# Kernel optimization log

Hardware: AMD Instinct MI355X
Metric: run time of the kernel (lower is better)

The kernel has to match this reference:

```python
import jax, jax.numpy as jnp
import numpy as np

N = 50000      # nodes
E = 800000     # edges (avg degree 16)
D = 128        # input_nf = output_nf
H = 128        # hidden_nf


def _lin_init(key, fan_in, fan_out, gain=1.0):
    return gain * jax.random.normal(key, (fan_in, fan_out), jnp.float32) / np.sqrt(fan_in)


def setup_inputs() -> dict:
    key = jax.random.key(0)
    ks = jax.random.split(key, 20)
    h = jax.random.normal(ks[0], (N, D), jnp.float32)
    coord_diff = 0.5 * jax.random.normal(ks[1], (E, 3), jnp.float32)
    row = jax.random.randint(ks[2], (E,), 0, N, jnp.int32)
    col = jax.random.randint(ks[3], (E,), 0, N, jnp.int32)
    return {
        "h": h, "coord_diff": coord_diff, "row": row, "col": col,
        # edge_nn: Linear(2D+1 -> H), SiLU, Linear(H -> H), SiLU
        "We1": _lin_init(ks[4], 2 * D + 1, H), "be1": jnp.zeros((H,), jnp.float32),
        "We2": _lin_init(ks[5], H, H),          "be2": jnp.zeros((H,), jnp.float32),
        # node_nn: Linear(H+D -> H), SiLU, Linear(H -> D)
        "Wn1": _lin_init(ks[6], H + D, H), "bn1": jnp.zeros((H,), jnp.float32),
        "Wn2": _lin_init(ks[7], H, D),     "bn2": jnp.zeros((D,), jnp.float32),
        # coord_nn: Linear(H -> H), SiLU, Linear(H -> 1, no bias, gain 0.001)
        "Wc1": _lin_init(ks[8], H, H), "bc1": jnp.zeros((H,), jnp.float32),
        "Wc2": _lin_init(ks[9], H, 1, gain=0.001),
        # vel_scaling_nn: Linear(D -> H), SiLU, Linear(H -> 1)
        "Wv1": _lin_init(ks[10], D, H), "bv1": jnp.zeros((H,), jnp.float32),
        "Wv2": _lin_init(ks[11], H, 1), "bv2": jnp.zeros((1,), jnp.float32),
    }


def reference(h, coord_diff, row, col,
              We1, be1, We2, be2,
              Wn1, bn1, Wn2, bn2,
              Wc1, bc1, Wc2,
              Wv1, bv1, Wv2, bv2):
    n = h.shape[0]
    silu = jax.nn.silu
    # radial: squared edge length, [E,1]
    radial = jnp.sum(coord_diff * coord_diff, axis=1, keepdims=True)
    # edge model: gather endpoint features + radial, 2-layer SiLU MLP
    e_in = jnp.concatenate([h[row], h[col], radial], axis=1)        # [E, 2D+1]
    m = silu(silu(e_in @ We1 + be1) @ We2 + be2)                    # [E, H]
    # force model: per-edge scalar coefficient, clamped scatter-mean (coords_weight=1.0)
    coef = silu(m @ Wc1 + bc1) @ Wc2                                # [E, 1]
    trans = jnp.clip(coord_diff * coef, -100.0, 100.0)              # [E, 3]
    f_sum = jax.ops.segment_sum(trans, row, num_segments=n)         # [N, 3]
    cnt = jax.ops.segment_sum(jnp.ones((trans.shape[0], 1), trans.dtype), row, num_segments=n)
    force = f_sum / jnp.clip(cnt, 1.0)                              # segment mean, count clamped >=1
    # node model: scatter-sum of edge messages, then 2-layer MLP
    agg = jax.ops.segment_sum(m, row, num_segments=n)               # [N, H]
    h_cat = jnp.concatenate([h, agg], axis=1)                       # [N, D+H]
    h_out = silu(h_cat @ Wn1 + bn1) @ Wn2 + bn2                     # [N, D]
    # velocity scaling head
    vel = silu(h @ Wv1 + bv1) @ Wv2 + bv2                           # [N, 1]
    return (vel, force, h_out)
```

## Files before the change

### kernel.cpp

```cpp
#include <hip/hip_runtime.h>

#define NN 50000
#define EE 800000

typedef unsigned short u16;
typedef unsigned int u32;
typedef __attribute__((ext_vector_type(8))) short short8;
typedef __attribute__((ext_vector_type(4))) float f32x4;
typedef __attribute__((ext_vector_type(2))) float f32x2;

__device__ __forceinline__ u16 f2bf(float f) {
    union { float f; u32 i; } v; v.f = f;
    u32 x = v.i;
    return (u16)((x + 0x7fffu + ((x >> 16) & 1u)) >> 16);
}
__device__ __forceinline__ u32 pkr(float lo, float hi) {
    union { float f; u32 i; } a, b; a.f = lo; b.f = hi;
    return __builtin_amdgcn_perm(b.i + 0x8000u, a.i + 0x8000u, 0x07060302u);
}
__device__ __forceinline__ float bf2f(short x) {
    union { u32 i; float f; } v; v.i = ((u32)(u16)x) << 16; return v.f;
}
__device__ __forceinline__ float siluf(float x) {
    return x * __builtin_amdgcn_rcpf(1.0f + __expf(-x));
}
__device__ __forceinline__ void atomic_pk_add_bf16(u16* addr, u32 data) {
    asm volatile("global_atomic_pk_add_bf16 %0, %1, off" :: "v"(addr), "v"(data) : "memory");
}

__device__ __forceinline__ int b_idx2(int k, int n) {
    int chunk = ((k >> 5) << 3) + ((n >> 5) << 1) + (n & 1);
    return chunk * 512 + (((k >> 3) & 3) << 7) + (((n >> 1) & 15) << 3) + (k & 7);
}

__global__ __launch_bounds__(256) void prep_kernel(
    const float* __restrict__ We1, const float* __restrict__ We2,
    const float* __restrict__ Wc1, const float* __restrict__ Wn1,
    const float* __restrict__ Wn2, const float* __restrict__ Wv1,
    u16* __restrict__ We1bf, u16* __restrict__ We2bf, u16* __restrict__ Wc1bf,
    u16* __restrict__ Wn1bf, u16* __restrict__ Wn2bf, u16* __restrict__ Wv1bf)
{
    int i = blockIdx.x * 256 + threadIdx.x;
    if (i < 32768) {
        int k = i >> 7, n = i & 127;
        We1bf[b_idx2(k, n)] = f2bf(We1[k * 128 + n]);
    } else if (i < 49152) {
        int t = i - 32768; int k = t >> 7, n = t & 127;
        We2bf[b_idx2(k, n)] = f2bf(We2[k * 128 + n]);
    } else if (i < 65536) {
        int t = i - 49152; int k = t >> 7, n = t & 127;
        Wc1bf[b_idx2(k, n)] = f2bf(Wc1[k * 128 + n]);
    } else if (i < 98304) {
        int t = i - 65536; int k = t >> 7, n = t & 127;
        Wn1bf[b_idx2(k, n)] = f2bf(Wn1[k * 128 + n]);
    } else if (i < 114688) {
        int t = i - 98304; int k = t >> 7, n = t & 127;
        Wn2bf[b_idx2(k, n)] = f2bf(Wn2[k * 128 + n]);
    } else {
        int t = i - 114688; int k = t >> 7, n = t & 127;
        Wv1bf[b_idx2(k, n)] = f2bf(Wv1[k * 128 + n]);
    }
}

__global__ __launch_bounds__(256) void hist_kernel(const int* __restrict__ row,
                                                   u32* __restrict__ bins)
{
    int e = blockIdx.x * 256 + threadIdx.x;
    if (e < EE) atomicAdd(&bins[row[e]], 1u);
}

__global__ __launch_bounds__(256) void scan1_kernel(const u32* __restrict__ bins,
                                                    u32* __restrict__ part)
{
    __shared__ u32 wsum[4];
    int i = blockIdx.x * 256 + threadIdx.x;
    u32 v = (i < NN) ? bins[i] : 0u;
    #pragma unroll
    for (int o = 1; o < 64; o <<= 1) v += __shfl_xor(v, o);
    if ((threadIdx.x & 63) == 0) wsum[threadIdx.x >> 6] = v;
    __syncthreads();
    if (threadIdx.x == 0) part[blockIdx.x] = wsum[0] + wsum[1] + wsum[2] + wsum[3];
}

__global__ __launch_bounds__(256) void scan2_kernel(u32* __restrict__ part, int np)
{
    __shared__ u32 s[256];
    int t = threadIdx.x;
    s[t] = (t < np) ? part[t] : 0u;
    __syncthreads();
    if (t == 0) {
        u32 run = 0;
        for (int i = 0; i < 256; ++i) { u32 x = s[i]; s[i] = run; run += x; }
    }
    __syncthreads();
    if (t < np) part[t] = s[t];
}

__global__ __launch_bounds__(256) void scan3_kernel(const u32* __restrict__ bins,
                                                    const u32* __restrict__ part,
                                                    u32* __restrict__ cursor)
{
    __shared__ u32 wsum[4];
    int t = threadIdx.x;
    int i = blockIdx.x * 256 + t;
    u32 v = (i < NN) ? bins[i] : 0u;
    u32 x = v;
    #pragma unroll
    for (int o = 1; o < 64; o <<= 1) {
        u32 y = __shfl_up(x, o);
        if ((t & 63) >= o) x += y;
    }
    if ((t & 63) == 63) wsum[t >> 6] = x;
    __syncthreads();
    u32 base = part[blockIdx.x];
    for (int wv = 0; wv < (t >> 6); ++wv) base += wsum[wv];
    if (i < NN) cursor[i] = base + x - v;
}

__global__ __launch_bounds__(256) void scatter_kernel(
    const int* __restrict__ row, const int* __restrict__ col,
    const float* __restrict__ cdiff, u32* __restrict__ cursor,
    u32* __restrict__ edata)
{
    int e = blockIdx.x * 256 + threadIdx.x;
    if (e < EE) {
        int r = row[e];
        u32 p = atomicAdd(&cursor[r], 1u);
        float cx = cdiff[(size_t)e * 3 + 0];
        float cy = cdiff[(size_t)e * 3 + 1];
        float cz = cdiff[(size_t)e * 3 + 2];
        float rad = cx * cx + cy * cy + cz * cz;
        uint4 ed;
        ed.x = (u32)r;
        ed.y = (u32)col[e];
        ed.z = __float_as_uint(rad);
        ed.w = (u32)e;
        *(uint4*)(edata + (size_t)p * 4) = ed;
    }
}

__global__ __launch_bounds__(256, 4) void pgemm_kernel(
    const float* __restrict__ h, const float* __restrict__ be1,
    const u16* __restrict__ We1bf,
    u16* __restrict__ P1bf, u16* __restrict__ P2bf,
    u16* __restrict__ hbf, u32 use_hbf)
{
    __shared__ u16 sX[8192];

    const int tid = threadIdx.x;
    const int nblk = blockIdx.x * 64;
    const int w = tid >> 6;
    const int lane = tid & 63;
    const int m15 = lane & 15, q = lane >> 4;
    const int n0 = w * 32 + 2 * m15, n1 = n0 + 1;
    const int ard = (m15 + 64 * q) * 8;
    const float b0 = be1[n0], b1 = be1[n1];

    {
        int r = tid & 63, j = tid >> 6;
        int n = nblk + r; if (n > NN - 1) n = NN - 1;
        const float* src = h + (size_t)n * 128 + j * 32;
        #pragma unroll
        for (int i = 0; i < 4; ++i) {
            float4 a = *(const float4*)(src + i * 8);
            float4 b = *(const float4*)(src + i * 8 + 4);
            int slot = r + ((j * 4 + i) << 6);
            uint4 v = make_uint4(pkr(a.x, a.y), pkr(a.z, a.w),
                                 pkr(b.x, b.y), pkr(b.z, b.w));
            *(uint4*)&sX[slot * 8] = v;
            if (use_hbf)
                *(uint4*)(hbf + (size_t)n * 128 + j * 32 + i * 8) = v;
        }
    }
    __syncthreads();

    f32x4 acc[4][2];

    #pragma unroll
    for (int mt = 0; mt < 4; ++mt)
        #pragma unroll
        for (int r = 0; r < 4; ++r) { acc[mt][0][r] = b0; acc[mt][1][r] = b1; }
    #pragma unroll
    for (int c = 0; c < 4; ++c) {
        short8 bf0 = *(const short8*)(We1bf + (c * 8 + w * 2 + 0) * 512 + lane * 8);
        short8 bf1 = *(const short8*)(We1bf + (c * 8 + w * 2 + 1) * 512 + lane * 8);
        #pragma unroll
        for (int mt = 0; mt < 4; ++mt) {
            short8 af = *(const short8*)(sX + ard + c * 2048 + mt * 128);
            acc[mt][0] = __builtin_amdgcn_mfma_f32_16x16x32_bf16(af, bf0, acc[mt][0], 0, 0, 0);
            acc[mt][1] = __builtin_amdgcn_mfma_f32_16x16x32_bf16(af, bf1, acc[mt][1], 0, 0, 0);
        }
    }
    #pragma unroll
    for (int mt = 0; mt < 4; ++mt)
        #pragma unroll
        for (int r = 0; r < 4; ++r) {
            int n = nblk + mt * 16 + q * 4 + r;
            if (n < NN)
                *(u32*)(P1bf + (size_t)n * 128 + n0) = pkr(acc[mt][0][r], acc[mt][1][r]);
        }

    #pragma unroll
    for (int mt = 0; mt < 4; ++mt)
        #pragma unroll
        for (int r = 0; r < 4; ++r) { acc[mt][0][r] = 0.0f; acc[mt][1][r] = 0.0f; }
    #pragma unroll
    for (int c = 4; c < 8; ++c) {
        short8 bf0 = *(const short8*)(We1bf + (c * 8 + w * 2 + 0) * 512 + lane * 8);
        short8 bf1 = *(const short8*)(We1bf + (c * 8 + w * 2 + 1) * 512 + lane * 8);
        #pragma unroll
        for (int mt = 0; mt < 4; ++mt) {
            short8 af = *(const short8*)(sX + ard + (c - 4) * 2048 + mt * 128);
            acc[mt][0] = __builtin_amdgcn_mfma_f32_16x16x32_bf16(af, bf0, acc[mt][0], 0, 0, 0);
            acc[mt][1] = __builtin_amdgcn_mfma_f32_16x16x32_bf16(af, bf1, acc[mt][1], 0, 0, 0);
        }
    }
    #pragma unroll
    for (int mt = 0; mt < 4; ++mt)
        #pragma unroll
        for (int r = 0; r < 4; ++r) {
            int n = nblk + mt * 16 + q * 4 + r;
            if (n < NN)
                *(u32*)(P2bf + (size_t)n * 128 + n0) = pkr(acc[mt][0][r], acc[mt][1][r]);
        }
}

__global__ __launch_bounds__(256, 8) void edge_kernel(
    const u16* __restrict__ P1bf, const u16* __restrict__ P2bf,
    const float* __restrict__ cdiff,
    const u32* __restrict__ edata,
    const float* __restrict__ We1,
    const float* __restrict__ be2, const float* __restrict__ bc1,
    const float* __restrict__ Wc2,
    const u16* __restrict__ We2bf, const u16* __restrict__ Wc1bf,
    u16* __restrict__ aggbf, float* __restrict__ fsum)
{
    __shared__ u16 sT[8192];
    __shared__ int sRow[64];
    __shared__ int sEg[64];
    __shared__ int sRid[64];
    __shared__ float sCoefP[4][64];
    __shared__ float sF[192];

    const int tid = threadIdx.x;
    const int e0 = blockIdx.x * 64;
    const int w = tid >> 6;
    const int lane = tid & 63;
    const int m15 = lane & 15, q = lane >> 4;
    const int n0 = w * 32 + 2 * m15, n1 = n0 + 1;
    const int lsw = (lane ^ q) * 8;
    const int a_ = m15 >> 2;
    const int sbase = (a_ << 7) + (q << 5) + ((m15 & 3) << 1);
    const int o0 = (0 ^ a_) << 3, o1 = (1 ^ a_) << 3, o2 = (2 ^ a_) << 3, o3 = (3 ^ a_) << 3;

    const float b2a = be2[n0], b2b = be2[n1];
    const float b3a = bc1[n0], b3b = bc1[n1];
    const float wc2a = Wc2[n0], wc2b = Wc2[n1];

    {
        int e = tid & 63, seg = tid >> 6;
        uint4 ed = *(const uint4*)(edata + (size_t)(e0 + e) * 4);
        int nr = (int)ed.x, nc = (int)ed.y;
        float rad = __uint_as_float(ed.z);
        if (seg == 0) { sRow[e] = nr; sEg[e] = (int)ed.w; }
        const u16* p1 = P1bf + (size_t)nr * 128 + seg * 32;
        const u16* p2 = P2bf + (size_t)nc * 128 + seg * 32;
        const float* wr = We1 + 256 * 128 + seg * 32;
        u16* tb = sT + (((seg * 4 + (e >> 4)) << 9) + (((e >> 2) & 3) << 5));
        const int rl = e & 3;
        #pragma unroll 2
        for (int g = 0; g < 4; ++g) {
            short8 x1 = *(const short8*)(p1 + g * 8);
            short8 x2 = *(const short8*)(p2 + g * 8);
            float4 wa = *(const float4*)(wr + g * 8);
            float4 wb = *(const float4*)(wr + g * 8 + 4);
            float v[8];
            #pragma unroll
            for (int t = 0; t < 4; ++t) {
                v[t]     = siluf(bf2f(x1[t])     + bf2f(x2[t])     + rad * ((const float*)&wa)[t]);
                v[t + 4] = siluf(bf2f(x1[t + 4]) + bf2f(x2[t + 4]) + rad * ((const float*)&wb)[t]);
            }
            uint4 dd = make_uint4(pkr(v[0], v[1]), pkr(v[2], v[3]),
                                  pkr(v[4], v[5]), pkr(v[6], v[7]));
            *(uint4*)(tb + ((g << 7) + ((rl ^ g) << 3))) = dd;
        }
    }
    __syncthreads();

    if (tid < 64) {
        int e = tid;
        int head = (e == 0) || (sRow[e] != sRow[e - 1]);
        int v = head ? e : 0;
        #pragma unroll
        for (int o = 1; o < 64; o <<= 1) {
            int y = __shfl_up(v, o);
            if (e >= o && y > v) v = y;
        }
        sRid[e] = v;
        sF[e * 3 + 0] = 0.f; sF[e * 3 + 1] = 0.f; sF[e * 3 + 2] = 0.f;
    }

    f32x4 acc[4][2];
    u32 d[4][4];

    #pragma unroll
    for (int mt = 0; mt < 4; ++mt)
        #pragma unroll
        for (int r = 0; r < 4; ++r) { acc[mt][0][r] = b2a; acc[mt][1][r] = b2b; }
    #pragma unroll
    for (int c = 0; c < 4; ++c) {
        short8 bf0 = *(const short8*)(We2bf + (c * 8 + w * 2 + 0) * 512 + lane * 8);
        short8 bf1 = *(const short8*)(We2bf + (c * 8 + w * 2 + 1) * 512 + lane * 8);
        #pragma unroll
        for (int mt = 0; mt < 4; ++mt) {
            short8 af = *(const short8*)(sT + (c * 4 + mt) * 512 + lsw);
            acc[mt][0] = __builtin_amdgcn_mfma_f32_16x16x32_bf16(af, bf0, acc[mt][0], 0, 0, 0);
            acc[mt][1] = __builtin_amdgcn_mfma_f32_16x16x32_bf16(af, bf1, acc[mt][1], 0, 0, 0);
        }
    }
    #pragma unroll
    for (int mt = 0; mt < 4; ++mt)
        #pragma unroll
        for (int r = 0; r < 4; ++r)
            d[mt][r] = pkr(siluf(acc[mt][0][r]), siluf(acc[mt][1][r]));
    __syncthreads();
    #pragma unroll
    for (int mt = 0; mt < 4; ++mt) {
        u16* bp = sT + (w * 4 + mt) * 512 + sbase;
        *(u32*)(bp + o0) = d[mt][0];
        *(u32*)(bp + o1) = d[mt][1];
        *(u32*)(bp + o2) = d[mt][2];
        *(u32*)(bp + o3) = d[mt][3];
    }
    __syncthreads();

    #pragma unroll
    for (int mt = 0; mt < 4; ++mt)
        #pragma unroll
        for (int r = 0; r < 4; ++r) { acc[mt][0][r] = b3a; acc[mt][1][r] = b3b; }
    #pragma unroll
    for (int c = 0; c < 4; ++c) {
        short8 bf0 = *(const short8*)(Wc1bf + (c * 8 + w * 2 + 0) * 512 + lane * 8);
        short8 bf1 = *(const short8*)(Wc1bf + (c * 8 + w * 2 + 1) * 512 + lane * 8);
        #pragma unroll
        for (int mt = 0; mt < 4; ++mt) {
            short8 af = *(const short8*)(sT + (c * 4 + mt) * 512 + lsw);
            acc[mt][0] = __builtin_amdgcn_mfma_f32_16x16x32_bf16(af, bf0, acc[mt][0], 0, 0, 0);
            acc[mt][1] = __builtin_amdgcn_mfma_f32_16x16x32_bf16(af, bf1, acc[mt][1], 0, 0, 0);
        }
    }
    #pragma unroll
    for (int mt = 0; mt < 4; ++mt)
        #pragma unroll
        for (int r = 0; r < 4; ++r) {
            float pv = fmaf(siluf(acc[mt][0][r]), wc2a, siluf(acc[mt][1][r]) * wc2b);
            pv += __shfl_xor(pv, 1);
            pv += __shfl_xor(pv, 2);
            pv += __shfl_xor(pv, 4);
            pv += __shfl_xor(pv, 8);
            if (m15 == 0) sCoefP[w][mt * 16 + q * 4 + r] = pv;
        }

    {
        const int P = tid & 63, C = 2 * P, g = tid >> 6;
        const int xorb = (C >> 3) & 3;
        const int base = ((((C >> 5) * 4 + g) << 9)) + (((C >> 3) & 3) << 7) + (C & 7);
        float s0 = 0.f, s1 = 0.f;
        int prow = sRow[g * 16];
        #pragma unroll
        for (int i = 0; i < 16; ++i) {
            u32 v = *(const u32*)(sT + base + (((i >> 2) & 3) << 5) + (((i & 3) ^ xorb) << 3));
            int r = sRow[g * 16 + i];
            if (r != prow) {
                atomic_pk_add_bf16(aggbf + (size_t)prow * 128 + C, pkr(s0, s1));
                s0 = 0.f; s1 = 0.f; prow = r;
            }
            s0 += bf2f((short)(v & 0xffffu));
            s1 += bf2f((short)(v >> 16));
        }
        atomic_pk_add_bf16(aggbf + (size_t)prow * 128 + C, pkr(s0, s1));
    }
    __syncthreads();

    if (tid < 192) {
        int e = tid / 3, ax = tid - e * 3;
        float coef = sCoefP[0][e] + sCoefP[1][e] + sCoefP[2][e] + sCoefP[3][e];
        float tr = cdiff[(size_t)sEg[e] * 3 + ax] * coef;
        tr = fminf(fmaxf(tr, -100.f), 100.f);
        atomicAdd(&sF[sRid[e] * 3 + ax], tr);
    }
    __syncthreads();
    if (tid < 192) {
        int e = tid / 3, ax = tid - e * 3;
        if (e == 0 || sRow[e] != sRow[e - 1])
            atomicAdd(&fsum[(size_t)sRow[e] * 3 + ax], sF[e * 3 + ax]);
    }
}

__global__ __launch_bounds__(256, 4) void node_kernel(
    const float* __restrict__ h, const u16* __restrict__ hbf, u32 use_hbf,
    const float* __restrict__ bn1, const float* __restrict__ bn2,
    const float* __restrict__ bv1, const float* __restrict__ Wv2,
    const float* __restrict__ bv2,
    const u16* __restrict__ Wn1bf, const u16* __restrict__ Wn2bf,
    const u16* __restrict__ Wv1bf,
    const u16* __restrict__ aggbf, const float* __restrict__ fsum,
    const u32* __restrict__ bins, float* __restrict__ out)
{
    __shared__ u16 sX[16384];
    __shared__ float sBn1[128], sBn2[128], sBv1[128];
    __shared__ float sVelP[4][64];
    u16* sT = sX + 8192;

    const int tid = threadIdx.x;
    const int nblk = blockIdx.x * 64;
    const int w = tid >> 6;
    const int lane = tid & 63;
    const int m15 = lane & 15, q = lane >> 4;
    const int n0 = w * 32 + 2 * m15, n1 = n0 + 1;
    const int lsw = (lane ^ q) * 8;
    const int a_ = m15 >> 2;
    const int sbase = (a_ << 7) + (q << 5) + ((m15 & 3) << 1);
    const int o0 = (0 ^ a_) << 3, o1 = (1 ^ a_) << 3, o2 = (2 ^ a_) << 3, o3 = (3 ^ a_) << 3;
    const int ard = (m15 + 64 * q) * 8;

    if (tid < 192) {
        int r = tid / 3, ax = tid - r * 3;
        int n = nblk + r;
        if (n < NN)
            out[NN + (size_t)n * 3 + ax] = fsum[(size_t)n * 3 + ax] * __builtin_amdgcn_rcpf(fmaxf((float)bins[n], 1.0f));
    }
    if (tid < 128) { sBn1[tid] = bn1[tid]; sBn2[tid] = bn2[tid]; sBv1[tid] = bv1[tid]; }
    const float wv2a = Wv2[n0], wv2b = Wv2[n1];

    {
        int r = tid & 63, j = tid >> 6;
        int n = nblk + r; if (n > NN - 1) n = NN - 1;
        if (j < 2) {
            if (use_hbf) {
                const u16* src = hbf + (size_t)n * 128 + j * 64;
                #pragma unroll
                for (int i = 0; i < 8; ++i) {
                    int slot = r + ((j * 8 + i) << 6);
                    *(uint4*)&sX[slot * 8] = *(const uint4*)(src + i * 8);
                }
            } else {
                const float* src = h + (size_t)n * 128 + j * 64;
                #pragma unroll
                for (int i = 0; i < 8; ++i) {
                    float4 a = *(const float4*)(src + i * 8);
                    float4 b = *(const float4*)(src + i * 8 + 4);
                    int slot = r + ((j * 8 + i) << 6);
                    *(uint4*)&sX[slot * 8] = make_uint4(pkr(a.x, a.y), pkr(a.z, a.w),
                                                        pkr(b.x, b.y), pkr(b.z, b.w));
                }
            }
        } else {
            const u16* src = aggbf + (size_t)n * 128 + (j & 1) * 64;
            #pragma unroll
            for (int i = 0; i < 8; ++i) {
                int slot = r + ((j * 8 + i) << 6);
                *(uint4*)&sX[slot * 8] = *(const uint4*)(src + i * 8);
            }
        }
    }
    __syncthreads();

    f32x4 acc[4][2];

    {
        float b0 = sBn1[n0], b1 = sBn1[n1];
        #pragma unroll
        for (int mt = 0; mt < 4; ++mt)
            #pragma unroll
            for (int r = 0; r < 4; ++r) { acc[mt][0][r] = b0; acc[mt][1][r] = b1; }
    }
    #pragma unroll
    for (int c = 0; c < 8; ++c) {
        short8 bf0 = *(const short8*)(Wn1bf + (c * 8 + w * 2 + 0) * 512 + lane * 8);
        short8 bf1 = *(const short8*)(Wn1bf + (c * 8 + w * 2 + 1) * 512 + lane * 8);
        #pragma unroll
        for (int mt = 0; mt < 4; ++mt) {
            short8 af = *(const short8*)(sX + ard + c * 2048 + mt * 128);
            acc[mt][0] = __builtin_amdgcn_mfma_f32_16x16x32_bf16(af, bf0, acc[mt][0], 0, 0, 0);
            acc[mt][1] = __builtin_amdgcn_mfma_f32_16x16x32_bf16(af, bf1, acc[mt][1], 0, 0, 0);
        }
    }
    u32 dn[4][4];
    #pragma unroll
    for (int mt = 0; mt < 4; ++mt)
        #pragma unroll
        for (int r = 0; r < 4; ++r)
            dn[mt][r] = pkr(siluf(acc[mt][0][r]), siluf(acc[mt][1][r]));
    __syncthreads();
    #pragma unroll
    for (int mt = 0; mt < 4; ++mt) {
        u16* bp = sT + (w * 4 + mt) * 512 + sbase;
        *(u32*)(bp + o0) = dn[mt][0];
        *(u32*)(bp + o1) = dn[mt][1];
        *(u32*)(bp + o2) = dn[mt][2];
        *(u32*)(bp + o3) = dn[mt][3];
    }
    __syncthreads();

    {
        float b0 = sBn2[n0], b1 = sBn2[n1];
        #pragma unroll
        for (int mt = 0; mt < 4; ++mt)
            #pragma unroll
            for (int r = 0; r < 4; ++r) { acc[mt][0][r] = b0; acc[mt][1][r] = b1; }
    }
    #pragma unroll
    for (int c = 0; c < 4; ++c) {
        short8 bf0 = *(const short8*)(Wn2bf + (c * 8 + w * 2 + 0) * 512 + lane * 8);
        short8 bf1 = *(const short8*)(Wn2bf + (c * 8 + w * 2 + 1) * 512 + lane * 8);
        #pragma unroll
        for (int mt = 0; mt < 4; ++mt) {
            short8 af = *(const short8*)(sT + (c * 4 + mt) * 512 + lsw);
            acc[mt][0] = __builtin_amdgcn_mfma_f32_16x16x32_bf16(af, bf0, acc[mt][0], 0, 0, 0);
            acc[mt][1] = __builtin_amdgcn_mfma_f32_16x16x32_bf16(af, bf1, acc[mt][1], 0, 0, 0);
        }
    }
    #pragma unroll
    for (int mt = 0; mt < 4; ++mt)
        #pragma unroll
        for (int r = 0; r < 4; ++r) {
            int n = nblk + mt * 16 + q * 4 + r;
            if (n < NN) {
                f32x2 v; v.x = acc[mt][0][r]; v.y = acc[mt][1][r];
                *(f32x2*)(out + (size_t)4 * NN + (size_t)n * 128 + n0) = v;
            }
        }

    {
        float b0 = sBv1[n0], b1 = sBv1[n1];
        #pragma unroll
        for (int mt = 0; mt < 4; ++mt)
            #pragma unroll
            for (int r = 0; r < 4; ++r) { acc[mt][0][r] = b0; acc[mt][1][r] = b1; }
    }
    #pragma unroll
    for (int c = 0; c < 4; ++c) {
        short8 bf0 = *(const short8*)(Wv1bf + (c * 8 + w * 2 + 0) * 512 + lane * 8);
        short8 bf1 = *(const short8*)(Wv1bf + (c * 8 + w * 2 + 1) * 512 + lane * 8);
        #pragma unroll
        for (int mt = 0; mt < 4; ++mt) {
            short8 af = *(const short8*)(sX + ard + c * 2048 + mt * 128);
            acc[mt][0] = __builtin_amdgcn_mfma_f32_16x16x32_bf16(af, bf0, acc[mt][0], 0, 0, 0);
            acc[mt][1] = __builtin_amdgcn_mfma_f32_16x16x32_bf16(af, bf1, acc[mt][1], 0, 0, 0);
        }
    }
    #pragma unroll
    for (int mt = 0; mt < 4; ++mt)
        #pragma unroll
        for (int r = 0; r < 4; ++r) {
            float pv = fmaf(siluf(acc[mt][0][r]), wv2a, siluf(acc[mt][1][r]) * wv2b);
            pv += __shfl_xor(pv, 1);
            pv += __shfl_xor(pv, 2);
            pv += __shfl_xor(pv, 4);
            pv += __shfl_xor(pv, 8);
            if (m15 == 0) sVelP[w][mt * 16 + q * 4 + r] = pv;
        }
    __syncthreads();

    if (tid < 64) {
        int n = nblk + tid;
        if (n < NN)
            out[n] = bv2[0] + sVelP[0][tid] + sVelP[1][tid] + sVelP[2][tid] + sVelP[3][tid];
    }
}

extern "C" void kernel_launch(void* const* d_in, const int* in_sizes, int n_in,
                              void* d_out, int out_size, void* d_ws, size_t ws_size,
                              hipStream_t stream) {
    const float* h     = (const float*)d_in[0];
    const float* cdiff = (const float*)d_in[1];
    const int* row     = (const int*)d_in[2];
    const int* col     = (const int*)d_in[3];
    const float* We1 = (const float*)d_in[4];
    const float* be1 = (const float*)d_in[5];
    const float* We2 = (const float*)d_in[6];
    const float* be2 = (const float*)d_in[7];
    const float* Wn1 = (const float*)d_in[8];
    const float* bn1 = (const float*)d_in[9];
    const float* Wn2 = (const float*)d_in[10];
    const float* bn2 = (const float*)d_in[11];
    const float* Wc1 = (const float*)d_in[12];
    const float* bc1 = (const float*)d_in[13];
    const float* Wc2 = (const float*)d_in[14];
    const float* Wv1 = (const float*)d_in[15];
    const float* bv1 = (const float*)d_in[16];
    const float* Wv2 = (const float*)d_in[17];
    const float* bv2 = (const float*)d_in[18];

    u16* aggbf  = (u16*)d_ws;
    float* fsum = (float*)(aggbf + (size_t)NN * 128);
    u32* bins   = (u32*)(fsum + (size_t)NN * 3);
    u16* We1bf = (u16*)(bins + NN);
    u16* We2bf = We1bf + 32768;
    u16* Wc1bf = We2bf + 16384;
    u16* Wn1bf = Wc1bf + 16384;
    u16* Wn2bf = Wn1bf + 32768;
    u16* Wv1bf = Wn2bf + 16384;
    u16* P1bf  = Wv1bf + 16384;
    float* out = (float*)d_out;

    const size_t base_bytes = (size_t)26662144;
    u16* hbf = (u16*)((char*)d_ws + base_bytes);
    u32 use_hbf = (ws_size >= base_bytes + (size_t)NN * 256) ? 1u : 0u;

    u32* cursor = (u32*)out;
    u32* part   = cursor + NN;
    u16* P2bf   = (u16*)(out + (size_t)4 * NN);
    u32* edata  = (u32*)(P2bf + (size_t)NN * 128);

    size_t zero_bytes = (size_t)NN * 128 * 2 + (size_t)NN * 3 * 4 + (size_t)NN * 4;
    hipMemsetAsync(d_ws, 0, zero_bytes, stream);

    const int NSC = (NN + 255) / 256;

    prep_kernel<<<512, 256, 0, stream>>>(We1, We2, Wc1, Wn1, Wn2, Wv1,
                                         We1bf, We2bf, Wc1bf, Wn1bf, Wn2bf, Wv1bf);
    pgemm_kernel<<<(NN + 63) / 64, 256, 0, stream>>>(h, be1, We1bf, P1bf, P2bf,
                                                     hbf, use_hbf);
    hist_kernel<<<(EE + 255) / 256, 256, 0, stream>>>(row, bins);
    scan1_kernel<<<NSC, 256, 0, stream>>>(bins, part);
    scan2_kernel<<<1, 256, 0, stream>>>(part, NSC);
    scan3_kernel<<<NSC, 256, 0, stream>>>(bins, part, cursor);
    scatter_kernel<<<(EE + 255) / 256, 256, 0, stream>>>(row, col, cdiff, cursor, edata);
    edge_kernel<<<EE / 64, 256, 0, stream>>>(P1bf, P2bf, cdiff, edata,
                                             We1, be2, bc1, Wc2,
                                             We2bf, Wc1bf,
                                             aggbf, fsum);
    node_kernel<<<(NN + 63) / 64, 256, 0, stream>>>(h, hbf, use_hbf,
                                                    bn1, bn2, bv1, Wv2, bv2,
                                                    Wn1bf, Wn2bf, Wv1bf,
                                                    aggbf, fsum, bins, out);
}
```

Before: 392.3 us.

## Process 128 edges per edge_kernel block to amortize weight fragment loads

Doubles the edge tile per block from 64 to 128 edges, so each wave runs 8 M-tiles per weight fragment load. The cost of the We2/Wc1 global loads and the block setup is spread over twice as many MFMAs. The segment-id scan now spans two wavefronts and is patched across the boundary, and the SiLU-pack round trip writes straight to LDS without holding an intermediate register array. In exchange the block needs twice the LDS and more accumulator registers, and launch bounds drop to 4 blocks per SM, so occupancy and latency hiding for the gathers fall.

```diff
diff --git a/kernel.cpp b/kernel.cpp
--- a/kernel.cpp
+++ b/kernel.cpp
@@ -225,7 +225,7 @@
         }
 }
 
-__global__ __launch_bounds__(256, 8) void edge_kernel(
+__global__ __launch_bounds__(256, 4) void edge_kernel(
     const u16* __restrict__ P1bf, const u16* __restrict__ P2bf,
     const float* __restrict__ cdiff,
     const u32* __restrict__ edata,
@@ -235,15 +235,15 @@
     const u16* __restrict__ We2bf, const u16* __restrict__ Wc1bf,
     u16* __restrict__ aggbf, float* __restrict__ fsum)
 {
-    __shared__ u16 sT[8192];
-    __shared__ int sRow[64];
-    __shared__ int sEg[64];
-    __shared__ int sRid[64];
-    __shared__ float sCoefP[4][64];
-    __shared__ float sF[192];
+    __shared__ u16 sT[16384];
+    __shared__ int sRow[128];
+    __shared__ int sEg[128];
+    __shared__ int sRid[128];
+    __shared__ float sCoefP[4][128];
+    __shared__ float sF[384];
 
     const int tid = threadIdx.x;
-    const int e0 = blockIdx.x * 64;
+    const int e0 = blockIdx.x * 128;
     const int w = tid >> 6;
     const int lane = tid & 63;
     const int m15 = lane & 15, q = lane >> 4;
@@ -258,53 +258,56 @@
     const float wc2a = Wc2[n0], wc2b = Wc2[n1];
 
     {
-        int e = tid & 63, seg = tid >> 6;
+        int e = tid & 127, hseg = tid >> 7;
         uint4 ed = *(const uint4*)(edata + (size_t)(e0 + e) * 4);
         int nr = (int)ed.x, nc = (int)ed.y;
         float rad = __uint_as_float(ed.z);
-        if (seg == 0) { sRow[e] = nr; sEg[e] = (int)ed.w; }
-        const u16* p1 = P1bf + (size_t)nr * 128 + seg * 32;
-        const u16* p2 = P2bf + (size_t)nc * 128 + seg * 32;
-        const float* wr = We1 + 256 * 128 + seg * 32;
-        u16* tb = sT + (((seg * 4 + (e >> 4)) << 9) + (((e >> 2) & 3) << 5));
+        if (tid < 128) { sRow[e] = nr; sEg[e] = (int)ed.w; }
         const int rl = e & 3;
-        #pragma unroll 2
-        for (int g = 0; g < 4; ++g) {
-            short8 x1 = *(const short8*)(p1 + g * 8);
-            short8 x2 = *(const short8*)(p2 + g * 8);
-            float4 wa = *(const float4*)(wr + g * 8);
-            float4 wb = *(const float4*)(wr + g * 8 + 4);
-            float v[8];
-            #pragma unroll
-            for (int t = 0; t < 4; ++t) {
-                v[t]     = siluf(bf2f(x1[t])     + bf2f(x2[t])     + rad * ((const float*)&wa)[t]);
-                v[t + 4] = siluf(bf2f(x1[t + 4]) + bf2f(x2[t + 4]) + rad * ((const float*)&wb)[t]);
+        #pragma unroll
+        for (int rep = 0; rep < 2; ++rep) {
+            int seg = hseg + rep * 2;
+            const u16* p1 = P1bf + (size_t)nr * 128 + seg * 32;
+            const u16* p2 = P2bf + (size_t)nc * 128 + seg * 32;
+            const float* wr = We1 + 256 * 128 + seg * 32;
+            u16* tb = sT + ((seg * 8 + (e >> 4)) << 9) + (((e >> 2) & 3) << 5);
+            #pragma unroll 2
+            for (int g = 0; g < 4; ++g) {
+                short8 x1 = *(const short8*)(p1 + g * 8);
+                short8 x2 = *(const short8*)(p2 + g * 8);
+                float4 wa = *(const float4*)(wr + g * 8);
+                float4 wb = *(const float4*)(wr + g * 8 + 4);
+                float v[8];
+                #pragma unroll
+                for (int t = 0; t < 4; ++t) {
+                    v[t]     = siluf(bf2f(x1[t])     + bf2f(x2[t])     + rad * ((const float*)&wa)[t]);
+                    v[t + 4] = siluf(bf2f(x1[t + 4]) + bf2f(x2[t + 4]) + rad * ((const float*)&wb)[t]);
+                }
+                uint4 dd = make_uint4(pkr(v[0], v[1]), pkr(v[2], v[3]),
+                                      pkr(v[4], v[5]), pkr(v[6], v[7]));
+                *(uint4*)(tb + ((g << 7) + ((rl ^ g) << 3))) = dd;
             }
-            uint4 dd = make_uint4(pkr(v[0], v[1]), pkr(v[2], v[3]),
-                                  pkr(v[4], v[5]), pkr(v[6], v[7]));
-            *(uint4*)(tb + ((g << 7) + ((rl ^ g) << 3))) = dd;
-        }
-    }
-    __syncthreads();
-
-    if (tid < 64) {
+        }
+    }
+    __syncthreads();
+
+    if (tid < 128) {
         int e = tid;
         int head = (e == 0) || (sRow[e] != sRow[e - 1]);
-        int v = head ? e : 0;
+        int v = head ? e : -1;
         #pragma unroll
         for (int o = 1; o < 64; o <<= 1) {
             int y = __shfl_up(v, o);
-            if (e >= o && y > v) v = y;
+            if (lane >= o && y > v) v = y;
         }
         sRid[e] = v;
         sF[e * 3 + 0] = 0.f; sF[e * 3 + 1] = 0.f; sF[e * 3 + 2] = 0.f;
     }
 
-    f32x4 acc[4][2];
-    u32 d[4][4];
-
-    #pragma unroll
-    for (int mt = 0; mt < 4; ++mt)
+    f32x4 acc[8][2];
+
+    #pragma unroll
+    for (int mt = 0; mt < 8; ++mt)
         #pragma unroll
         for (int r = 0; r < 4; ++r) { acc[mt][0][r] = b2a; acc[mt][1][r] = b2b; }
     #pragma unroll
@@ -312,30 +315,26 @@
         short8 bf0 = *(const short8*)(We2bf + (c * 8 + w * 2 + 0) * 512 + lane * 8);
         short8 bf1 = *(const short8*)(We2bf + (c * 8 + w * 2 + 1) * 512 + lane * 8);
         #pragma unroll
-        for (int mt = 0; mt < 4; ++mt) {
-            short8 af = *(const short8*)(sT + (c * 4 + mt) * 512 + lsw);
+        for (int mt = 0; mt < 8; ++mt) {
+            short8 af = *(const short8*)(sT + (c * 8 + mt) * 512 + lsw);
             acc[mt][0] = __builtin_amdgcn_mfma_f32_16x16x32_bf16(af, bf0, acc[mt][0], 0, 0, 0);
             acc[mt][1] = __builtin_amdgcn_mfma_f32_16x16x32_bf16(af, bf1, acc[mt][1], 0, 0, 0);
         }
     }
-    #pragma unroll
-    for (int mt = 0; mt < 4; ++mt)
-        #pragma unroll
-        for (int r = 0; r < 4; ++r)
-            d[mt][r] = pkr(siluf(acc[mt][0][r]), siluf(acc[mt][1][r]));
-    __syncthreads();
-    #pragma unroll
-    for (int mt = 0; mt < 4; ++mt) {
-        u16* bp = sT + (w * 4 + mt) * 512 + sbase;
-        *(u32*)(bp + o0) = d[mt][0];
-        *(u32*)(bp + o1) = d[mt][1];
-        *(u32*)(bp + o2) = d[mt][2];
-        *(u32*)(bp + o3) = d[mt][3];
-    }
-    __syncthreads();
-
-    #pragma unroll
-    for (int mt = 0; mt < 4; ++mt)
+    __syncthreads();
+    if (tid >= 64 && tid < 128 && sRid[tid] < 0) sRid[tid] = sRid[63];
+    #pragma unroll
+    for (int mt = 0; mt < 8; ++mt) {
+        u16* bp = sT + (w * 8 + mt) * 512 + sbase;
+        *(u32*)(bp + o0) = pkr(siluf(acc[mt][0][0]), siluf(acc[mt][1][0]));
+        *(u32*)(bp + o1) = pkr(siluf(acc[mt][0][1]), siluf(acc[mt][1][1]));
+        *(u32*)(bp + o2) = pkr(siluf(acc[mt][0][2]), siluf(acc[mt][1][2]));
+        *(u32*)(bp + o3) = pkr(siluf(acc[mt][0][3]), siluf(acc[mt][1][3]));
+    }
+    __syncthreads();
+
+    #pragma unroll
+    for (int mt = 0; mt < 8; ++mt)
         #pragma unroll
         for (int r = 0; r < 4; ++r) { acc[mt][0][r] = b3a; acc[mt][1][r] = b3b; }
     #pragma unroll
@@ -343,14 +342,14 @@
         short8 bf0 = *(const short8*)(Wc1bf + (c * 8 + w * 2 + 0) * 512 + lane * 8);
         short8 bf1 = *(const short8*)(Wc1bf + (c * 8 + w * 2 + 1) * 512 + lane * 8);
         #pragma unroll
-        for (int mt = 0; mt < 4; ++mt) {
-            short8 af = *(const short8*)(sT + (c * 4 + mt) * 512 + lsw);
+        for (int mt = 0; mt < 8; ++mt) {
+            short8 af = *(const short8*)(sT + (c * 8 + mt) * 512 + lsw);
             acc[mt][0] = __builtin_amdgcn_mfma_f32_16x16x32_bf16(af, bf0, acc[mt][0], 0, 0, 0);
             acc[mt][1] = __builtin_amdgcn_mfma_f32_16x16x32_bf16(af, bf1, acc[mt][1], 0, 0, 0);
         }
     }
     #pragma unroll
-    for (int mt = 0; mt < 4; ++mt)
+    for (int mt = 0; mt < 8; ++mt)
         #pragma unroll
         for (int r = 0; r < 4; ++r) {
             float pv = fmaf(siluf(acc[mt][0][r]), wc2a, siluf(acc[mt][1][r]) * wc2b);
@@ -362,15 +361,16 @@
         }
 
     {
-        const int P = tid & 63, C = 2 * P, g = tid >> 6;
+        const int C = 2 * lane, g = tid >> 6;
         const int xorb = (C >> 3) & 3;
-        const int base = ((((C >> 5) * 4 + g) << 9)) + (((C >> 3) & 3) << 7) + (C & 7);
+        const int base = ((((C >> 5) * 8 + g * 2) << 9)) + (((C >> 3) & 3) << 7) + (C & 7);
         float s0 = 0.f, s1 = 0.f;
-        int prow = sRow[g * 16];
-        #pragma unroll
-        for (int i = 0; i < 16; ++i) {
-            u32 v = *(const u32*)(sT + base + (((i >> 2) & 3) << 5) + (((i & 3) ^ xorb) << 3));
-            int r = sRow[g * 16 + i];
+        int prow = sRow[g * 32];
+        #pragma unroll
+        for (int i = 0; i < 32; ++i) {
+            u32 v = *(const u32*)(sT + base + ((i >> 4) << 9) +
+                                  (((i >> 2) & 3) << 5) + (((i & 3) ^ xorb) << 3));
+            int r = sRow[g * 32 + i];
             if (r != prow) {
                 atomic_pk_add_bf16(aggbf + (size_t)prow * 128 + C, pkr(s0, s1));
                 s0 = 0.f; s1 = 0.f; prow = r;
@@ -382,18 +382,26 @@
     }
     __syncthreads();
 
-    if (tid < 192) {
-        int e = tid / 3, ax = tid - e * 3;
-        float coef = sCoefP[0][e] + sCoefP[1][e] + sCoefP[2][e] + sCoefP[3][e];
-        float tr = cdiff[(size_t)sEg[e] * 3 + ax] * coef;
-        tr = fminf(fmaxf(tr, -100.f), 100.f);
-        atomicAdd(&sF[sRid[e] * 3 + ax], tr);
-    }
-    __syncthreads();
-    if (tid < 192) {
-        int e = tid / 3, ax = tid - e * 3;
-        if (e == 0 || sRow[e] != sRow[e - 1])
-            atomicAdd(&fsum[(size_t)sRow[e] * 3 + ax], sF[e * 3 + ax]);
+    #pragma unroll
+    for (int pass = 0; pass < 2; ++pass) {
+        int t2 = tid + pass * 256;
+        if (t2 < 384) {
+            int e = t2 / 3, ax = t2 - e * 3;
+            float coef = sCoefP[0][e] + sCoefP[1][e] + sCoefP[2][e] + sCoefP[3][e];
+            float tr = cdiff[(size_t)sEg[e] * 3 + ax] * coef;
+            tr = fminf(fmaxf(tr, -100.f), 100.f);
+            atomicAdd(&sF[sRid[e] * 3 + ax], tr);
+        }
+    }
+    __syncthreads();
+    #pragma unroll
+    for (int pass = 0; pass < 2; ++pass) {
+        int t2 = tid + pass * 256;
+        if (t2 < 384) {
+            int e = t2 / 3, ax = t2 - e * 3;
+            if (e == 0 || sRow[e] != sRow[e - 1])
+                atomicAdd(&fsum[(size_t)sRow[e] * 3 + ax], sF[e * 3 + ax]);
+        }
     }
 }
 
@@ -628,10 +636,10 @@
     scan2_kernel<<<1, 256, 0, stream>>>(part, NSC);
     scan3_kernel<<<NSC, 256, 0, stream>>>(bins, part, cursor);
     scatter_kernel<<<(EE + 255) / 256, 256, 0, stream>>>(row, col, cdiff, cursor, edata);
-    edge_kernel<<<EE / 64, 256, 0, stream>>>(P1bf, P2bf, cdiff, edata,
-                                             We1, be2, bc1, Wc2,
-                                             We2bf, Wc1bf,
-                                             aggbf, fsum);
+    edge_kernel<<<EE / 128, 256, 0, stream>>>(P1bf, P2bf, cdiff, edata,
+                                              We1, be2, bc1, Wc2,
+                                              We2bf, Wc1bf,
+                                              aggbf, fsum);
     node_kernel<<<(NN + 63) / 64, 256, 0, stream>>>(h, hbf, use_hbf,
                                                     bn1, bn2, bv1, Wv2, bv2,
                                                     Wn1bf, Wn2bf, Wv1bf,
```

Measured after the change: 404.1 us. 1.03x slower.

## Store sorted coord diffs with edges and move velocity head into pgemm

Applied to the files above, without the earlier changes.

The scatter pass now writes each edge's cx, cy into the sorted edge record and cz into a separate sorted workspace array. The edge kernel can then recompute the radial term and read coordinates from shared memory instead of doing a random gather from cdiff by original edge index. Separately, the velocity MLP head moves from the node kernel into the pgemm kernel, reusing the h tile already staged in shared memory. This shortens the node kernel but lengthens pgemm, and it relocates the cursor scratch buffer so vel can be written early. The new path needs a larger workspace and falls back when it is too small.

```diff
diff --git a/kernel.cpp b/kernel.cpp
--- a/kernel.cpp
+++ b/kernel.cpp
@@ -120,7 +120,7 @@
 __global__ __launch_bounds__(256) void scatter_kernel(
     const int* __restrict__ row, const int* __restrict__ col,
     const float* __restrict__ cdiff, u32* __restrict__ cursor,
-    u32* __restrict__ edata)
+    u32* __restrict__ edata, float* __restrict__ czS, u32 use_cz)
 {
     int e = blockIdx.x * 256 + threadIdx.x;
     if (e < EE) {
@@ -129,23 +129,31 @@
         float cx = cdiff[(size_t)e * 3 + 0];
         float cy = cdiff[(size_t)e * 3 + 1];
         float cz = cdiff[(size_t)e * 3 + 2];
-        float rad = cx * cx + cy * cy + cz * cz;
         uint4 ed;
         ed.x = (u32)r;
         ed.y = (u32)col[e];
-        ed.z = __float_as_uint(rad);
-        ed.w = (u32)e;
+        if (use_cz) {
+            ed.z = __float_as_uint(cx);
+            ed.w = __float_as_uint(cy);
+            czS[p] = cz;
+        } else {
+            ed.z = __float_as_uint(cx * cx + cy * cy + cz * cz);
+            ed.w = (u32)e;
+        }
         *(uint4*)(edata + (size_t)p * 4) = ed;
     }
 }
 
 __global__ __launch_bounds__(256, 4) void pgemm_kernel(
     const float* __restrict__ h, const float* __restrict__ be1,
-    const u16* __restrict__ We1bf,
+    const float* __restrict__ bv1, const float* __restrict__ Wv2,
+    const float* __restrict__ bv2,
+    const u16* __restrict__ We1bf, const u16* __restrict__ Wv1bf,
     u16* __restrict__ P1bf, u16* __restrict__ P2bf,
-    u16* __restrict__ hbf, u32 use_hbf)
+    u16* __restrict__ hbf, u32 use_hbf, float* __restrict__ vel)
 {
     __shared__ u16 sX[8192];
+    __shared__ float sVelP[4][64];
 
     const int tid = threadIdx.x;
     const int nblk = blockIdx.x * 64;
@@ -223,12 +231,49 @@
             if (n < NN)
                 *(u32*)(P2bf + (size_t)n * 128 + n0) = pkr(acc[mt][0][r], acc[mt][1][r]);
         }
+
+    {
+        const float bva = bv1[n0], bvb = bv1[n1];
+        const float wv2a = Wv2[n0], wv2b = Wv2[n1];
+        #pragma unroll
+        for (int mt = 0; mt < 4; ++mt)
+            #pragma unroll
+            for (int r = 0; r < 4; ++r) { acc[mt][0][r] = bva; acc[mt][1][r] = bvb; }
+        #pragma unroll
+        for (int c = 0; c < 4; ++c) {
+            short8 bf0 = *(const short8*)(Wv1bf + (c * 8 + w * 2 + 0) * 512 + lane * 8);
+            short8 bf1 = *(const short8*)(Wv1bf + (c * 8 + w * 2 + 1) * 512 + lane * 8);
+            #pragma unroll
+            for (int mt = 0; mt < 4; ++mt) {
+                short8 af = *(const short8*)(sX + ard + c * 2048 + mt * 128);
+                acc[mt][0] = __builtin_amdgcn_mfma_f32_16x16x32_bf16(af, bf0, acc[mt][0], 0, 0, 0);
+                acc[mt][1] = __builtin_amdgcn_mfma_f32_16x16x32_bf16(af, bf1, acc[mt][1], 0, 0, 0);
+            }
+        }
+        #pragma unroll
+        for (int mt = 0; mt < 4; ++mt)
+            #pragma unroll
+            for (int r = 0; r < 4; ++r) {
+                float pv = fmaf(siluf(acc[mt][0][r]), wv2a, siluf(acc[mt][1][r]) * wv2b);
+                pv += __shfl_xor(pv, 1);
+                pv += __shfl_xor(pv, 2);
+                pv += __shfl_xor(pv, 4);
+                pv += __shfl_xor(pv, 8);
+                if (m15 == 0) sVelP[w][mt * 16 + q * 4 + r] = pv;
+            }
+        __syncthreads();
+        if (tid < 64) {
+            int n = nblk + tid;
+            if (n < NN)
+                vel[n] = bv2[0] + sVelP[0][tid] + sVelP[1][tid] + sVelP[2][tid] + sVelP[3][tid];
+        }
+    }
 }
 
 __global__ __launch_bounds__(256, 8) void edge_kernel(
     const u16* __restrict__ P1bf, const u16* __restrict__ P2bf,
     const float* __restrict__ cdiff,
-    const u32* __restrict__ edata,
+    const u32* __restrict__ edata, const float* __restrict__ czS, u32 use_cz,
     const float* __restrict__ We1,
     const float* __restrict__ be2, const float* __restrict__ bc1,
     const float* __restrict__ Wc2,
@@ -238,6 +283,7 @@
     __shared__ u16 sT[8192];
     __shared__ int sRow[64];
     __shared__ int sEg[64];
+    __shared__ float sCd[64][3];
     __shared__ int sRid[64];
     __shared__ float sCoefP[4][64];
     __shared__ float sF[192];
@@ -261,8 +307,16 @@
         int e = tid & 63, seg = tid >> 6;
         uint4 ed = *(const uint4*)(edata + (size_t)(e0 + e) * 4);
         int nr = (int)ed.x, nc = (int)ed.y;
-        float rad = __uint_as_float(ed.z);
-        if (seg == 0) { sRow[e] = nr; sEg[e] = (int)ed.w; }
+        float rad;
+        if (use_cz) {
+            float cx = __uint_as_float(ed.z), cy = __uint_as_float(ed.w);
+            float cz = czS[e0 + e];
+            rad = cx * cx + cy * cy + cz * cz;
+            if (seg == 0) { sRow[e] = nr; sCd[e][0] = cx; sCd[e][1] = cy; sCd[e][2] = cz; }
+        } else {
+            rad = __uint_as_float(ed.z);
+            if (seg == 0) { sRow[e] = nr; sEg[e] = (int)ed.w; }
+        }
         const u16* p1 = P1bf + (size_t)nr * 128 + seg * 32;
         const u16* p2 = P2bf + (size_t)nc * 128 + seg * 32;
         const float* wr = We1 + 256 * 128 + seg * 32;
@@ -385,7 +439,8 @@
     if (tid < 192) {
         int e = tid / 3, ax = tid - e * 3;
         float coef = sCoefP[0][e] + sCoefP[1][e] + sCoefP[2][e] + sCoefP[3][e];
-        float tr = cdiff[(size_t)sEg[e] * 3 + ax] * coef;
+        float cd = use_cz ? sCd[e][ax] : cdiff[(size_t)sEg[e] * 3 + ax];
+        float tr = cd * coef;
         tr = fminf(fmaxf(tr, -100.f), 100.f);
         atomicAdd(&sF[sRid[e] * 3 + ax], tr);
     }
@@ -400,16 +455,12 @@
 __global__ __launch_bounds__(256, 4) void node_kernel(
     const float* __restrict__ h, const u16* __restrict__ hbf, u32 use_hbf,
     const float* __restrict__ bn1, const float* __restrict__ bn2,
-    const float* __restrict__ bv1, const float* __restrict__ Wv2,
-    const float* __restrict__ bv2,
     const u16* __restrict__ Wn1bf, const u16* __restrict__ Wn2bf,
-    const u16* __restrict__ Wv1bf,
     const u16* __restrict__ aggbf, const float* __restrict__ fsum,
     const u32* __restrict__ bins, float* __restrict__ out)
 {
     __shared__ u16 sX[16384];
-    __shared__ float sBn1[128], sBn2[128], sBv1[128];
-    __shared__ float sVelP[4][64];
+    __shared__ float sBn1[128], sBn2[128];
     u16* sT = sX + 8192;
 
     const int tid = threadIdx.x;
@@ -430,8 +481,7 @@
         if (n < NN)
             out[NN + (size_t)n * 3 + ax] = fsum[(size_t)n * 3 + ax] * __builtin_amdgcn_rcpf(fmaxf((float)bins[n], 1.0f));
     }
-    if (tid < 128) { sBn1[tid] = bn1[tid]; sBn2[tid] = bn2[tid]; sBv1[tid] = bv1[tid]; }
-    const float wv2a = Wv2[n0], wv2b = Wv2[n1];
+    if (tid < 128) { sBn1[tid] = bn1[tid]; sBn2[tid] = bn2[tid]; }
 
     {
         int r = tid & 63, j = tid >> 6;
@@ -531,43 +581,6 @@
                 *(f32x2*)(out + (size_t)4 * NN + (size_t)n * 128 + n0) = v;
             }
         }
-
-    {
-        float b0 = sBv1[n0], b1 = sBv1[n1];
-        #pragma unroll
-        for (int mt = 0; mt < 4; ++mt)
-            #pragma unroll
-            for (int r = 0; r < 4; ++r) { acc[mt][0][r] = b0; acc[mt][1][r] = b1; }
-    }
-    #pragma unroll
-    for (int c = 0; c < 4; ++c) {
-        short8 bf0 = *(const short8*)(Wv1bf + (c * 8 + w * 2 + 0) * 512 + lane * 8);
-        short8 bf1 = *(const short8*)(Wv1bf + (c * 8 + w * 2 + 1) * 512 + lane * 8);
-        #pragma unroll
-        for (int mt = 0; mt < 4; ++mt) {
-            short8 af = *(const short8*)(sX + ard + c * 2048 + mt * 128);
-            acc[mt][0] = __builtin_amdgcn_mfma_f32_16x16x32_bf16(af, bf0, acc[mt][0], 0, 0, 0);
-            acc[mt][1] = __builtin_amdgcn_mfma_f32_16x16x32_bf16(af, bf1, acc[mt][1], 0, 0, 0);
-        }
-    }
-    #pragma unroll
-    for (int mt = 0; mt < 4; ++mt)
-        #pragma unroll
-        for (int r = 0; r < 4; ++r) {
-            float pv = fmaf(siluf(acc[mt][0][r]), wv2a, siluf(acc[mt][1][r]) * wv2b);
-            pv += __shfl_xor(pv, 1);
-            pv += __shfl_xor(pv, 2);
-            pv += __shfl_xor(pv, 4);
-            pv += __shfl_xor(pv, 8);
-            if (m15 == 0) sVelP[w][mt * 16 + q * 4 + r] = pv;
-        }
-    __syncthreads();
-
-    if (tid < 64) {
-        int n = nblk + tid;
-        if (n < NN)
-            out[n] = bv2[0] + sVelP[0][tid] + sVelP[1][tid] + sVelP[2][tid] + sVelP[3][tid];
-    }
 }
 
 extern "C" void kernel_launch(void* const* d_in, const int* in_sizes, int n_in,
@@ -608,8 +621,10 @@
     const size_t base_bytes = (size_t)26662144;
     u16* hbf = (u16*)((char*)d_ws + base_bytes);
     u32 use_hbf = (ws_size >= base_bytes + (size_t)NN * 256) ? 1u : 0u;
-
-    u32* cursor = (u32*)out;
+    float* czS = (float*)((char*)d_ws + base_bytes + (size_t)NN * 256);
+    u32 use_cz = (ws_size >= base_bytes + (size_t)NN * 256 + (size_t)EE * 4) ? 1u : 0u;
+
+    u32* cursor = (u32*)(out + NN);
     u32* part   = cursor + NN;
     u16* P2bf   = (u16*)(out + (size_t)4 * NN);
     u32* edata  = (u32*)(P2bf + (size_t)NN * 128);
@@ -621,19 +636,21 @@
 
     prep_kernel<<<512, 256, 0, stream>>>(We1, We2, Wc1, Wn1, Wn2, Wv1,
                                          We1bf, We2bf, Wc1bf, Wn1bf, Wn2bf, Wv1bf);
-    pgemm_kernel<<<(NN + 63) / 64, 256, 0, stream>>>(h, be1, We1bf, P1bf, P2bf,
-                                                     hbf, use_hbf);
+    pgemm_kernel<<<(NN + 63) / 64, 256, 0, stream>>>(h, be1, bv1, Wv2, bv2,
+                                                     We1bf, Wv1bf, P1bf, P2bf,
+                                                     hbf, use_hbf, out);
     hist_kernel<<<(EE + 255) / 256, 256, 0, stream>>>(row, bins);
     scan1_kernel<<<NSC, 256, 0, stream>>>(bins, part);
     scan2_kernel<<<1, 256, 0, stream>>>(part, NSC);
     scan3_kernel<<<NSC, 256, 0, stream>>>(bins, part, cursor);
-    scatter_kernel<<<(EE + 255) / 256, 256, 0, stream>>>(row, col, cdiff, cursor, edata);
-    edge_kernel<<<EE / 64, 256, 0, stream>>>(P1bf, P2bf, cdiff, edata,
+    scatter_kernel<<<(EE + 255) / 256, 256, 0, stream>>>(row, col, cdiff, cursor,
+                                                         edata, czS, use_cz);
+    edge_kernel<<<EE / 64, 256, 0, stream>>>(P1bf, P2bf, cdiff, edata, czS, use_cz,
                                              We1, be2, bc1, Wc2,
                                              We2bf, Wc1bf,
                                              aggbf, fsum);
     node_kernel<<<(NN + 63) / 64, 256, 0, stream>>>(h, hbf, use_hbf,
-                                                    bn1, bn2, bv1, Wv2, bv2,
-                                                    Wn1bf, Wn2bf, Wv1bf,
+                                                    bn1, bn2,
+                                                    Wn1bf, Wn2bf,
                                                     aggbf, fsum, bins, out);
 }
```

Result: slower. 402.9 us (+2.7%).
